# Optimization experiments

Measured on AMD Instinct MI355X. Metric: run time of the kernel, lower is better.

The kernel has to match this reference:

```python
import jax, jax.numpy as jnp
import numpy as np

LEVELS = ((64, 176), (32, 88), (16, 44), (8, 22))
S_TOTAL = sum(h * w for h, w in LEVELS)  # 14960
C = 128; HH = 8; HD = 16; R = 4; L = 4; P = 8
G = 32; PC_MIN = -4.0; PC_MAX = 4.0
NUM_CLASSES = 17; PROP = 3 + 3 + 4 + 1 + NUM_CLASSES  # 28


def _ln(x, g, b):
    m = x.mean(-1, keepdims=True)
    v = ((x - m) ** 2).mean(-1, keepdims=True)
    return (x - m) * jax.lax.rsqrt(v + 1e-5) * g + b


def setup_inputs() -> dict:
    key = jax.random.key(0)
    ks = jax.random.split(key, 20)
    B, N, CAM = 1, 1024, 6
    d = {}
    d['query'] = jax.random.normal(ks[0], (B, N, C), jnp.float32)
    d['gaussian_props'] = jax.random.normal(ks[1], (B, N, PROP), jnp.float32)
    d['ms_feats'] = jax.random.normal(ks[2], (B, CAM, S_TOTAL, C), jnp.float32)
    d['depth_maps'] = jax.random.uniform(ks[3], (B, CAM, 64, 176), jnp.float32, 0.5, 50.0)
    d['lidar2img'] = jax.random.normal(ks[4], (B, CAM, 4, 4), jnp.float32)
    d['img_h'] = 256
    d['img_w'] = 704
    w = lambda k, shp: jax.random.normal(k, shp, jnp.float32) * 0.02
    d['W_sc'] = w(ks[5], (3, 3, 3, C, C)); d['b_sc'] = jnp.zeros((C,), jnp.float32)
    d['sc_g'] = jnp.ones((C,), jnp.float32); d['sc_b'] = jnp.zeros((C,), jnp.float32)
    d['ref_off_w'] = w(ks[6], (C, R * 3)); d['ref_off_b'] = jnp.zeros((R * 3,), jnp.float32)
    d['off_w'] = w(ks[7], (C, HH * R * L * P * 2)); d['off_b'] = jnp.zeros((HH * R * L * P * 2,), jnp.float32)
    d['aw_w'] = w(ks[8], (C, HH * R * L * P)); d['aw_b'] = jnp.zeros((HH * R * L * P,), jnp.float32)
    d['val_w'] = w(ks[9], (C, C)); d['val_b'] = jnp.zeros((C,), jnp.float32)
    d['out_w'] = w(ks[10], (C, C)); d['out_b'] = jnp.zeros((C,), jnp.float32)
    d['an_g'] = jnp.ones((C,), jnp.float32); d['an_b'] = jnp.zeros((C,), jnp.float32)
    d['f1_w'] = w(ks[11], (C, 4 * C)); d['f1_b'] = jnp.zeros((4 * C,), jnp.float32)
    d['f2_w'] = w(ks[12], (4 * C, C)); d['f2_b'] = jnp.zeros((C,), jnp.float32)
    d['fn_g'] = jnp.ones((C,), jnp.float32); d['fn_b'] = jnp.zeros((C,), jnp.float32)
    d['p1_w'] = w(ks[13], (C, C)); d['p1_b'] = jnp.zeros((C,), jnp.float32)
    d['p2_w'] = w(ks[14], (C, PROP)); d['p2_b'] = jnp.zeros((PROP,), jnp.float32)
    return d


def _forward(query, gaussian_props, ms_feats, depth_maps, lidar2img,
             W_sc, b_sc, sc_g, sc_b, ref_off_w, ref_off_b, off_w, off_b,
             aw_w, aw_b, val_w, val_b, out_w, out_b, an_g, an_b,
             f1_w, f1_b, f2_w, f2_b, fn_g, fn_b, p1_w, p1_b, p2_w, p2_b,
             img_h, img_w):
    B, N, _ = query.shape
    CAM = ms_feats.shape[1]
    means = gaussian_props[..., :3]
    # ---- SparseConv3DBlock: scatter-mean voxelization, 3x3x3 conv, gather back ----
    vs = (PC_MAX - PC_MIN) / G
    vox = jnp.clip(jnp.floor((means - PC_MIN) / vs).astype(jnp.int32), 0, G - 1)
    flat = (vox[..., 0] * G + vox[..., 1]) * G + vox[..., 2]  # [B,N]
    bi = jnp.arange(B)[:, None]
    grid = jnp.zeros((B, G * G * G, C), query.dtype).at[bi, flat].add(query)
    cnt = jnp.zeros((B, G * G * G, 1), query.dtype).at[bi, flat].add(1.0)
    grid = (grid / jnp.maximum(cnt, 1.0)).reshape(B, G, G, G, C)
    grid = jax.lax.conv_general_dilated(grid, W_sc, (1, 1, 1), 'SAME',
                                        dimension_numbers=('NDHWC', 'DHWIO', 'NDHWC')) + b_sc
    grid = jax.nn.gelu(grid).reshape(B, G * G * G, C)
    query = _ln(query + grid[bi, flat], sc_g, sc_b)
    # ---- DeformableAttention3D ----
    fW = jnp.asarray(img_w, query.dtype); fH = jnp.asarray(img_h, query.dtype)
    ref3d = means[:, :, None, :] + (query @ ref_off_w + ref_off_b).reshape(B, N, R, 3)
    pts = jnp.concatenate([ref3d, jnp.ones_like(ref3d[..., :1])], -1)
    proj = jnp.einsum('bcij,bnrj->bcnri', lidar2img, pts)  # [B,CAM,N,R,4]
    z = proj[..., 2]; zc = jnp.maximum(z, 1e-5)
    u = proj[..., 0] / zc; v = proj[..., 1] / zc
    valid = (z > 1e-5) & (u >= 0) & (u < fW) & (v >= 0) & (v < fH)
    Hd, Wd = depth_maps.shape[2], depth_maps.shape[3]
    iu = jnp.clip((u / fW * Wd).astype(jnp.int32), 0, Wd - 1)
    iv = jnp.clip((v / fH * Hd).astype(jnp.int32), 0, Hd - 1)
    ds = jnp.take_along_axis(depth_maps.reshape(B, CAM, Hd * Wd),
                             (iv * Wd + iu).reshape(B, CAM, N * R), axis=2).reshape(B, CAM, N, R)
    wmask = jnp.exp(-jnp.abs(z - ds)) * valid.astype(query.dtype)  # [B,CAM,N,R]
    ref2 = jnp.stack([u / fW, v / fH], -1)  # [B,CAM,N,R,2]
    offs = (query @ off_w + off_b).reshape(B, N, HH, R, L, P, 2)
    attn = jax.nn.softmax((query @ aw_w + aw_b).reshape(B, N, HH, R * L * P), -1)
    attn = attn.reshape(B, N, HH, R, L, P)
    value = (ms_feats @ val_w + val_b).reshape(B, CAM, S_TOTAL, HH, HD)
    out = jnp.zeros((B, N, HH, HD), query.dtype)
    s0 = 0
    for l, (Hl, Wl) in enumerate(LEVELS):
        sz = Hl * Wl
        vl = value[:, :, s0:s0 + sz].transpose(0, 1, 3, 2, 4).reshape(B * CAM, HH, sz, HD)
        s0 += sz
        off_l = offs[:, :, :, :, l]  # [B,N,HH,R,P,2]
        loc = ref2[:, :, :, None, :, None, :] + off_l[:, None] / jnp.array([Wl, Hl], query.dtype)
        # loc: [B,CAM,N,HH,R,P,2] in normalized coords
        x = (loc[..., 0] * Wl - 0.5).transpose(0, 1, 3, 2, 4, 5).reshape(B * CAM, HH, N * R * P)
        y = (loc[..., 1] * Hl - 0.5).transpose(0, 1, 3, 2, 4, 5).reshape(B * CAM, HH, N * R * P)
        x0 = jnp.floor(x); y0 = jnp.floor(y); wx = x - x0; wy = y - y0
        x0i = jnp.clip(x0.astype(jnp.int32), 0, Wl - 1)
        x1i = jnp.clip(x0.astype(jnp.int32) + 1, 0, Wl - 1)
        y0i = jnp.clip(y0.astype(jnp.int32), 0, Hl - 1)
        y1i = jnp.clip(y0.astype(jnp.int32) + 1, 0, Hl - 1)
        g = lambda ix, iy: jnp.take_along_axis(vl, (iy * Wl + ix)[..., None], axis=2)
        samp = (((1 - wx) * (1 - wy))[..., None] * g(x0i, y0i)
                + (wx * (1 - wy))[..., None] * g(x1i, y0i)
                + ((1 - wx) * wy)[..., None] * g(x0i, y1i)
                + (wx * wy)[..., None] * g(x1i, y1i))  # [B*CAM,HH,N*R*P,HD]
        samp = samp.reshape(B, CAM, HH, N, R, P, HD)
        ws = attn[:, :, :, :, l, :][:, None].transpose(0, 1, 3, 2, 4, 5) * wmask[:, :, None, :, :, None]
        out = out + jnp.einsum('bchnrp,bchnrpd->bnhd', ws, samp)
    attn_out = out.reshape(B, N, C) @ out_w + out_b
    query = _ln(query + attn_out, an_g, an_b)
    query = _ln(query + (jax.nn.gelu(query @ f1_w + f1_b) @ f2_w + f2_b), fn_g, fn_b)
    props = gaussian_props + (jax.nn.gelu(query @ p1_w + p1_b) @ p2_w + p2_b)
    return query, props


def reference(query, gaussian_props, ms_feats, depth_maps, lidar2img,
              W_sc, b_sc, sc_g, sc_b, ref_off_w, ref_off_b, off_w, off_b,
              aw_w, aw_b, val_w, val_b, out_w, out_b, an_g, an_b,
              f1_w, f1_b, f2_w, f2_b, fn_g, fn_b, p1_w, p1_b, p2_w, p2_b,
              img_h, img_w):
    return _forward(query, gaussian_props, ms_feats, depth_maps, lidar2img,
                    W_sc, b_sc, sc_g, sc_b, ref_off_w, ref_off_b, off_w, off_b,
                    aw_w, aw_b, val_w, val_b, out_w, out_b, an_g, an_b,
                    f1_w, f1_b, f2_w, f2_b, fn_g, fn_b, p1_w, p1_b, p2_w, p2_b,
                    img_h, img_w)
```

## Files before the change

kernel.cpp:

```cpp
#include <hip/hip_runtime.h>
#include <hip/hip_bf16.h>
#include <math.h>

#define NQ    1024
#define CC    128
#define CAM   6
#define RR    4
#define LL    4
#define PP    8
#define HHD   8
#define HDD   16
#define GG    32
#define S_TOT 14960
#define PROPN 28
#define NTAP  27
#define MVAL  (CAM * S_TOT)
#define NVB   ((MVAL + 63) / 64)
#define NCVB  (8 * NTAP)

typedef __attribute__((ext_vector_type(8))) short bf16x8;
typedef __attribute__((ext_vector_type(4))) float f32x4;

__device__ __forceinline__ float gelu_tanh(float x) {
    return 0.5f * x * (1.0f + tanhf(0.7978845608028654f * (x + 0.044715f * x * x * x)));
}

__device__ __forceinline__ unsigned short f2bf(float f) {
    union { float f; unsigned int u; } x; x.f = f;
    unsigned int r = (x.u + 0x7FFFu + ((x.u >> 16) & 1u)) >> 16;
    return (unsigned short)r;
}

__device__ __forceinline__ float bf2f(short s) {
    union { unsigned int u; float f; } x;
    x.u = ((unsigned int)(unsigned short)s) << 16;
    return x.f;
}

__global__ void k_wt_scatter(const float* __restrict__ Wsc, unsigned short* __restrict__ WscT,
                             const float* __restrict__ valw, unsigned short* __restrict__ valwT,
                             const float* __restrict__ outw, unsigned short* __restrict__ outwT,
                             const float* __restrict__ p1w, unsigned short* __restrict__ p1wT,
                             const float* __restrict__ f1w, unsigned short* __restrict__ f1wT,
                             const float* __restrict__ f2w, unsigned short* __restrict__ f2wT,
                             const float* __restrict__ offw, unsigned short* __restrict__ offwT,
                             const float* __restrict__ aww, unsigned short* __restrict__ awwT,
                             const float* __restrict__ p2w, unsigned short* __restrict__ p2wT,
                             const float* __restrict__ p2b, float* __restrict__ p2bp,
                             const float* __restrict__ qin, const float* __restrict__ gp,
                             float* __restrict__ grid, float* __restrict__ cnt,
                             int* __restrict__ flatidx) {
    __shared__ float t[64][65];
    __shared__ int sflat[2];
    int z = blockIdx.z;
    int tid = threadIdx.x;

    if (z >= 63) {
        int half = tid >> 7, c = tid & 127;
        int n = ((z - 63) * 4 + (blockIdx.x * 2 + blockIdx.y)) * 2 + half;
        if (c == 0) {
            float mx = gp[n * PROPN + 0], my = gp[n * PROPN + 1], mz = gp[n * PROPN + 2];
            int vx = (int)floorf((mx + 4.0f) * 4.0f);
            int vy = (int)floorf((my + 4.0f) * 4.0f);
            int vz = (int)floorf((mz + 4.0f) * 4.0f);
            vx = min(max(vx, 0), GG - 1);
            vy = min(max(vy, 0), GG - 1);
            vz = min(max(vz, 0), GG - 1);
            int f = (vx * GG + vy) * GG + vz;
            sflat[half] = f;
            flatidx[n] = f;
            atomicAdd(&cnt[f], 1.0f);
        }
        __syncthreads();
        atomicAdd(&grid[(size_t)sflat[half] * CC + c], qin[(size_t)n * CC + c]);
        return;
    }

    int n0 = blockIdx.x * 64, k0 = blockIdx.y * 64;
    if (z == 62) {
#pragma unroll
        for (int it = 0; it < 16; ++it) {
            int idx = tid + it * 256;
            int r = idx >> 6, c = idx & 63;
            t[r][c] = (n0 + c < PROPN) ? p2w[(size_t)(k0 + r) * PROPN + n0 + c] : 0.f;
        }
        __syncthreads();
#pragma unroll
        for (int it = 0; it < 16; ++it) {
            int idx = tid + it * 256;
            int r = idx >> 6, c = idx & 63;
            p2wT[(size_t)(n0 + r) * 128 + k0 + c] = f2bf(t[c][r]);
        }
        if (blockIdx.x == 0 && blockIdx.y == 0 && tid < 128)
            p2bp[tid] = (tid < PROPN) ? p2b[tid] : 0.f;
        return;
    }
    const float* src; unsigned short* dst; int ss, ds;
    if (z < 27)       { src = Wsc + (size_t)z * 16384; dst = WscT + (size_t)z * 16384; ss = 128; ds = 128; }
    else if (z == 27) { src = valw; dst = valwT; ss = 128; ds = 128; }
    else if (z == 28) { src = outw; dst = outwT; ss = 128; ds = 128; }
    else if (z == 29) { src = p1w;  dst = p1wT;  ss = 128; ds = 128; }
    else if (z < 34)  { int q = z - 30; src = f1w + q * 128; dst = f1wT + (size_t)q * 16384; ss = 512;  ds = 128; }
    else if (z < 38)  { int q = z - 34; src = f2w + (size_t)q * 16384; dst = f2wT + q * 128; ss = 128;  ds = 512; }
    else if (z < 54)  { int q = z - 38; src = offw + q * 128; dst = offwT + (size_t)q * 16384; ss = 2048; ds = 128; }
    else              { int q = z - 54; src = aww + q * 128;  dst = awwT + (size_t)q * 16384; ss = 1024; ds = 128; }
#pragma unroll
    for (int it = 0; it < 16; ++it) {
        int idx = tid + it * 256;
        int r = idx >> 6, c = idx & 63;
        t[r][c] = src[(size_t)(k0 + r) * ss + n0 + c];
    }
    __syncthreads();
#pragma unroll
    for (int it = 0; it < 16; ++it) {
        int idx = tid + it * 256;
        int r = idx >> 6, c = idx & 63;
        dst[(size_t)(n0 + r) * ds + k0 + c] = f2bf(t[c][r]);
    }
}

union CVSm {
    struct { bf16x8 As[128 * 16]; bf16x8 Bs[128 * 16]; } c;
    struct { bf16x8 Bs[128 * 16]; unsigned short Os[64 * 128]; float sbias[128]; } v;
};
__global__ __launch_bounds__(256) void k_conv_val(
    const float* __restrict__ grid, const float* __restrict__ cnt,
    const int* __restrict__ flatidx, const unsigned short* __restrict__ WT,
    float* __restrict__ convacc27,
    const float* __restrict__ ms, const unsigned short* __restrict__ valwT,
    const float* __restrict__ valb, unsigned short* __restrict__ value)
{
    __shared__ CVSm sm;
    __shared__ int   nbase[128];
    __shared__ float nscale[128];
    int bx = blockIdx.x, tid = threadIdx.x;
    int lane = tid & 63, wv = tid >> 6;
    int r = lane & 15, q = lane >> 4;

    if (bx >= NCVB) {
        int vb = bx - NCVB;
        int m0 = vb * 64;
#pragma unroll
        for (int it = 0; it < 8; ++it) {
            int idx = tid + it * 256;
            int n = idx >> 4, c = idx & 15;
            sm.v.Bs[n * 16 + (c ^ (n & 15))] = *(const bf16x8*)(valwT + (size_t)n * 128 + c * 8);
        }
        if (tid < 128) sm.v.sbias[tid] = valb[tid];
        __syncthreads();

        int row = m0 + wv * 16 + r;
        int mg = min(row, MVAL - 1);
        const float* pA = ms + (size_t)mg * 128;

        f32x4 acc[8];
#pragma unroll
        for (int j = 0; j < 8; ++j)
#pragma unroll
            for (int e = 0; e < 4; ++e) acc[j][e] = 0.f;

#pragma unroll
        for (int ks = 0; ks < 4; ++ks) {
            const float* p = pA + ks * 32 + q * 8;
            float4 aa = *(const float4*)p;
            float4 bb = *(const float4*)(p + 4);
            bf16x8 af;
            af[0] = (short)f2bf(aa.x); af[1] = (short)f2bf(aa.y);
            af[2] = (short)f2bf(aa.z); af[3] = (short)f2bf(aa.w);
            af[4] = (short)f2bf(bb.x); af[5] = (short)f2bf(bb.y);
            af[6] = (short)f2bf(bb.z); af[7] = (short)f2bf(bb.w);
            bf16x8 bfr[8];
#pragma unroll
            for (int j = 0; j < 8; ++j)
                bfr[j] = sm.v.Bs[(j * 16 + r) * 16 + ((ks * 4 + q) ^ r)];
#pragma unroll
            for (int j = 0; j < 8; ++j)
                acc[j] = __builtin_amdgcn_mfma_f32_16x16x32_bf16(af, bfr[j], acc[j], 0, 0, 0);
        }

#pragma unroll
        for (int j = 0; j < 8; ++j)
#pragma unroll
            for (int e = 0; e < 4; ++e) {
                int rl = wv * 16 + q * 4 + e;
                sm.v.Os[rl * 128 + j * 16 + r] = f2bf(acc[j][e] + sm.v.sbias[j * 16 + r]);
            }
        __syncthreads();
#pragma unroll
        for (int it = 0; it < 2; ++it) {
            int idx = tid + it * 256;
            int rl = idx & 63, h = idx >> 6;
            int m = m0 + rl;
            if (m < MVAL) {
                int cam = m / S_TOT;
                int s = m - cam * S_TOT;
                int pos, HW, sb;
                if (s < 11264)      { pos = s;          HW = 11264; sb = 0; }
                else if (s < 14080) { pos = s - 11264;  HW = 2816;  sb = 11264; }
                else if (s < 14784) { pos = s - 14080;  HW = 704;   sb = 14080; }
                else                { pos = s - 14784;  HW = 176;   sb = 14784; }
                size_t dst = ((size_t)cam * S_TOT + sb) * CC
                           + (size_t)h * (HW * HDD) + (size_t)pos * HDD;
                *(bf16x8*)(value + dst)     = *(const bf16x8*)&sm.v.Os[rl * 128 + h * 16];
                *(bf16x8*)(value + dst + 8) = *(const bf16x8*)&sm.v.Os[rl * 128 + h * 16 + 8];
            }
        }
        return;
    }

    int tap = bx >> 3;
    int q0 = (bx & 7) * 128;
    int dz = tap / 9 - 1, dy = (tap / 3) % 3 - 1, dx = tap % 3 - 1;

    if (tid < 128) {
        int f = flatidx[q0 + tid];
        int nx = (f >> 10) + dz, ny = ((f >> 5) & 31) + dy, nz = (f & 31) + dx;
        bool ok = (nx >= 0 && nx < GG && ny >= 0 && ny < GG && nz >= 0 && nz < GG);
        int nf = ok ? (nx * GG + ny) * GG + nz : 0;
        nbase[tid] = nf;
        nscale[tid] = ok ? 1.0f / fmaxf(cnt[nf], 1.0f) : 0.f;
    }
    __syncthreads();
#pragma unroll
    for (int it = 0; it < 8; ++it) {
        int idx = tid + it * 256;
        int m = idx >> 4, c = idx & 15;
        const float* p = grid + (size_t)nbase[m] * CC + c * 8;
        float s = nscale[m];
        float4 a = *(const float4*)p;
        float4 b = *(const float4*)(p + 4);
        bf16x8 u;
        u[0] = (short)f2bf(a.x * s); u[1] = (short)f2bf(a.y * s);
        u[2] = (short)f2bf(a.z * s); u[3] = (short)f2bf(a.w * s);
        u[4] = (short)f2bf(b.x * s); u[5] = (short)f2bf(b.y * s);
        u[6] = (short)f2bf(b.z * s); u[7] = (short)f2bf(b.w * s);
        sm.c.As[m * 16 + (c ^ (m & 15))] = u;
    }
    const unsigned short* Wt = WT + (size_t)tap * CC * CC;
#pragma unroll
    for (int it = 0; it < 8; ++it) {
        int idx = tid + it * 256;
        int n = idx >> 4, c = idx & 15;
        bf16x8 w = *(const bf16x8*)(Wt + (size_t)n * CC + c * 8);
        sm.c.Bs[n * 16 + (c ^ (n & 15))] = w;
    }
    __syncthreads();

    int wr = (wv >> 1) * 64, wc = (wv & 1) * 64;
    f32x4 acc[4][4];
#pragma unroll
    for (int i = 0; i < 4; ++i)
#pragma unroll
        for (int j = 0; j < 4; ++j)
#pragma unroll
            for (int e = 0; e < 4; ++e) acc[i][j][e] = 0.f;
#pragma unroll
    for (int ks = 0; ks < 4; ++ks) {
        bf16x8 bfr[4];
#pragma unroll
        for (int j = 0; j < 4; ++j)
            bfr[j] = sm.c.Bs[(wc + j * 16 + r) * 16 + ((ks * 4 + q) ^ r)];
#pragma unroll
        for (int i = 0; i < 4; ++i) {
            bf16x8 af = sm.c.As[(wr + i * 16 + r) * 16 + ((ks * 4 + q) ^ r)];
#pragma unroll
            for (int j = 0; j < 4; ++j)
                acc[i][j] = __builtin_amdgcn_mfma_f32_16x16x32_bf16(af, bfr[j], acc[i][j], 0, 0, 0);
        }
    }
    float* dst = convacc27 + (size_t)tap * NQ * CC;
#pragma unroll
    for (int i = 0; i < 4; ++i)
#pragma unroll
        for (int e = 0; e < 4; ++e) {
            int m = q0 + wr + i * 16 + q * 4 + e;
#pragma unroll
            for (int j = 0; j < 4; ++j) {
                int col = wc + j * 16 + r;
                dst[(size_t)m * CC + col] = acc[i][j][e];
            }
        }
}

__global__ void k_ln_conv_proj(const float* __restrict__ a, const float* __restrict__ convacc27,
                               const float* __restrict__ bconv,
                               const float* __restrict__ g, const float* __restrict__ be,
                               float* __restrict__ out, unsigned short* __restrict__ outbf,
                               const float* __restrict__ refw, const float* __restrict__ refb,
                               const float* __restrict__ gp, const float* __restrict__ l2i,
                               const float* __restrict__ depth,
                               const int* __restrict__ ih, const int* __restrict__ iw,
                               float* __restrict__ wm, float* __restrict__ r2u,
                               float* __restrict__ r2v) {
    int n = blockIdx.x, c = threadIdx.x;
    float apart = 0.f;
#pragma unroll
    for (int t = 0; t < NTAP; ++t) apart += convacc27[((size_t)t * NQ + n) * CC + c];
    float x = a[n * CC + c] + gelu_tanh(apart + bconv[c]);
    __shared__ float w4[4];
    __shared__ float qrow[CC];
    __shared__ float ro[12];
    float s = x;
#pragma unroll
    for (int d = 1; d < 64; d <<= 1) s += __shfl_xor(s, d);
    if ((c & 63) == 0) w4[c >> 6] = s;
    __syncthreads();
    float m = (w4[0] + w4[1]) * (1.0f / CC);
    float dd = x - m;
    float v = dd * dd;
#pragma unroll
    for (int d = 1; d < 64; d <<= 1) v += __shfl_xor(v, d);
    if ((c & 63) == 0) w4[2 + (c >> 6)] = v;
    __syncthreads();
    float var = (w4[2] + w4[3]) * (1.0f / CC);
    float qv = dd * rsqrtf(var + 1e-5f) * g[c] + be[c];
    out[n * CC + c] = qv;
    outbf[n * CC + c] = f2bf(qv);
    qrow[c] = qv;
    __syncthreads();
    if (c < 12) {
        float sacc = refb[c];
#pragma unroll 4
        for (int k = 0; k < 128; ++k) sacc += qrow[k] * refw[k * 12 + c];
        ro[c] = sacc;
    }
    __syncthreads();
    if (c < 24) {
        int cam = c >> 2, r = c & 3;
        float fH = (float)(*ih), fW = (float)(*iw);
        const float* M = l2i + cam * 16;
        float px = gp[n * PROPN + 0] + ro[r * 3 + 0];
        float py = gp[n * PROPN + 1] + ro[r * 3 + 1];
        float pz = gp[n * PROPN + 2] + ro[r * 3 + 2];
        float p0 = M[0] * px + M[1] * py + M[2]  * pz + M[3];
        float p1 = M[4] * px + M[5] * py + M[6]  * pz + M[7];
        float p2 = M[8] * px + M[9] * py + M[10] * pz + M[11];
        float zc = fmaxf(p2, 1e-5f);
        float u = p0 / zc, vv = p1 / zc;
        bool valid = (p2 > 1e-5f) && (u >= 0.f) && (u < fW) && (vv >= 0.f) && (vv < fH);
        int iu = min(max((int)(u / fW * 176.f), 0), 175);
        int iv = min(max((int)(vv / fH * 64.f), 0), 63);
        float ds = depth[cam * 64 * 176 + iv * 176 + iu];
        int o = cam * (NQ * RR) + n * RR + r;
        wm[o]  = valid ? expf(-fabsf(p2 - ds)) : 0.f;
        r2u[o] = u / fW;
        r2v[o] = vv / fH;
    }
}

__global__ __launch_bounds__(256) void k_qhead(
    const unsigned short* __restrict__ Abf,
    const unsigned short* __restrict__ offwT, const float* __restrict__ offb,
    unsigned short* __restrict__ offsb,
    const unsigned short* __restrict__ awwT, const float* __restrict__ awb,
    unsigned short* __restrict__ attn)
{
    __shared__ bf16x8 Bs[128 * 16];
    int bx = blockIdx.x, tid = threadIdx.x;
    int lane = tid & 63, wv = tid >> 6;
    int r = lane & 15, q = lane >> 4;
    bool isoff = bx < 16;
    int n0 = (isoff ? bx : (bx - 16)) * 128;
    const unsigned short* WT = isoff ? offwT : awwT;
    int m0 = blockIdx.y * 128;
    int mw = m0 + wv * 32;

#pragma unroll
    for (int it = 0; it < 8; ++it) {
        int idx = tid + it * 256;
        int n = idx >> 4, c = idx & 15;
        Bs[n * 16 + (c ^ (n & 15))] = *(const bf16x8*)(WT + (size_t)(n0 + n) * 128 + c * 8);
    }
    __syncthreads();

    f32x4 acc[2][8];
#pragma unroll
    for (int i = 0; i < 2; ++i)
#pragma unroll
        for (int j = 0; j < 8; ++j)
#pragma unroll
            for (int e = 0; e < 4; ++e) acc[i][j][e] = 0.f;

#pragma unroll
    for (int ks = 0; ks < 4; ++ks) {
        bf16x8 af[2];
#pragma unroll
        for (int i = 0; i < 2; ++i)
            af[i] = *(const bf16x8*)(Abf + (size_t)(mw + i * 16 + r) * 128 + (ks * 4 + q) * 8);
#pragma unroll
        for (int j = 0; j < 8; ++j) {
            bf16x8 b = Bs[(j * 16 + r) * 16 + ((ks * 4 + q) ^ r)];
#pragma unroll
            for (int i = 0; i < 2; ++i)
                acc[i][j] = __builtin_amdgcn_mfma_f32_16x16x32_bf16(af[i], b, acc[i][j], 0, 0, 0);
        }
    }

    float bia[8];
    const float* bsrc = isoff ? offb : awb;
#pragma unroll
    for (int j = 0; j < 8; ++j) bia[j] = bsrc[n0 + j * 16 + r];

    if (isoff) {
#pragma unroll
        for (int i = 0; i < 2; ++i)
#pragma unroll
            for (int e = 0; e < 4; ++e) {
                int m = mw + i * 16 + q * 4 + e;
                unsigned short* orow = offsb + (size_t)m * 2048 + n0;
#pragma unroll
                for (int j = 0; j < 8; ++j)
                    orow[j * 16 + r] = f2bf(acc[i][j][e] + bia[j]);
            }
    } else {
#pragma unroll
        for (int i = 0; i < 2; ++i)
#pragma unroll
            for (int e = 0; e < 4; ++e) {
                float mx = -1e30f;
#pragma unroll
                for (int j = 0; j < 8; ++j) mx = fmaxf(mx, acc[i][j][e] + bia[j]);
#pragma unroll
                for (int d = 1; d < 16; d <<= 1) mx = fmaxf(mx, __shfl_xor(mx, d));
                float ex[8];
                float sum = 0.f;
#pragma unroll
                for (int j = 0; j < 8; ++j) { ex[j] = expf(acc[i][j][e] + bia[j] - mx); sum += ex[j]; }
#pragma unroll
                for (int d = 1; d < 16; d <<= 1) sum += __shfl_xor(sum, d);
                float inv = 1.0f / sum;
                int m = mw + i * 16 + q * 4 + e;
                unsigned short* orow = attn + (size_t)m * 1024 + n0;
#pragma unroll
                for (int j = 0; j < 8; ++j)
                    orow[j * 16 + r] = f2bf(ex[j] * inv);
            }
    }
}

__global__ __launch_bounds__(512) void k_sample(
                         const unsigned short* __restrict__ value,
                         const unsigned short* __restrict__ offsb,
                         const unsigned short* __restrict__ attn,
                         const float* __restrict__ wm,
                         const float* __restrict__ r2u, const float* __restrict__ r2v,
                         float* __restrict__ sampout) {
    const int Wl_[4] = {176, 88, 44, 22};
    const int Hl_[4] = {64, 32, 16, 8};
    const int s0_[4] = {0, 11264, 14080, 14784};
    int n = blockIdx.x, tid = threadIdx.x;
    __shared__ float s_attn[1024];
    __shared__ float s_offs[2048];
    __shared__ float s_wm[24], s_ru[24], s_rv[24];
    __shared__ float part[HHD][HDD];

    if (tid < 128) {
        bf16x8 v = *(const bf16x8*)(attn + (size_t)n * 1024 + tid * 8);
#pragma unroll
        for (int d = 0; d < 8; ++d) s_attn[tid * 8 + d] = bf2f(v[d]);
    }
    if (tid < 256) {
        bf16x8 v = *(const bf16x8*)(offsb + (size_t)n * 2048 + tid * 8);
#pragma unroll
        for (int d = 0; d < 8; ++d) s_offs[tid * 8 + d] = bf2f(v[d]);
    }
    if (tid < 24) {
        int cam = tid >> 2, r = tid & 3;
        int o = cam * (NQ * RR) + n * RR + r;
        s_wm[tid] = wm[o]; s_ru[tid] = r2u[o]; s_rv[tid] = r2v[o];
    }
    __syncthreads();

    int half = tid >> 8;
    int t8 = tid & 255;
    int h = t8 >> 5, slot = t8 & 31;
    int l = slot >> 3, p = slot & 7;
    int Wl = Wl_[l], Hl = Hl_[l];
    float fWl = (float)Wl, fHl = (float)Hl;
    size_t planeC = (size_t)s0_[l] * CC + (size_t)h * (Hl * Wl * HDD);
    float acc[16];
#pragma unroll
    for (int d = 0; d < 16; ++d) acc[d] = 0.f;

    for (int cr = half * 12; cr < half * 12 + 12; ++cr) {
        int cam = cr >> 2, r = cr & 3;
        float ws = s_attn[h * 128 + r * 32 + l * 8 + p] * s_wm[cr];
        if (ws == 0.f) continue;
        float ox = s_offs[h * 256 + r * 64 + l * 16 + p * 2 + 0];
        float oy = s_offs[h * 256 + r * 64 + l * 16 + p * 2 + 1];
        float x = s_ru[cr] * fWl + ox - 0.5f;
        float y = s_rv[cr] * fHl + oy - 0.5f;
        float xf = floorf(x), yf = floorf(y);
        float wx = x - xf, wy = y - yf;
        int x0 = min(max((int)xf, 0), Wl - 1);
        int x1 = min(max((int)xf + 1, 0), Wl - 1);
        int y0 = min(max((int)yf, 0), Hl - 1);
        int y1 = min(max((int)yf + 1, 0), Hl - 1);
        const unsigned short* base = value + (size_t)cam * S_TOT * CC + planeC;
        const unsigned short* p00 = base + (size_t)(y0 * Wl + x0) * HDD;
        const unsigned short* p01 = base + (size_t)(y0 * Wl + x1) * HDD;
        const unsigned short* p10 = base + (size_t)(y1 * Wl + x0) * HDD;
        const unsigned short* p11 = base + (size_t)(y1 * Wl + x1) * HDD;
        float w00 = ws * (1.f - wx) * (1.f - wy);
        float w01 = ws * wx * (1.f - wy);
        float w10 = ws * (1.f - wx) * wy;
        float w11 = ws * wx * wy;
        bf16x8 va0 = *(const bf16x8*)p00, va1 = *(const bf16x8*)(p00 + 8);
        bf16x8 vb0 = *(const bf16x8*)p01, vb1 = *(const bf16x8*)(p01 + 8);
        bf16x8 vc0 = *(const bf16x8*)p10, vc1 = *(const bf16x8*)(p10 + 8);
        bf16x8 vd0 = *(const bf16x8*)p11, vd1 = *(const bf16x8*)(p11 + 8);
#pragma unroll
        for (int d = 0; d < 8; ++d)
            acc[d] += w00 * bf2f(va0[d]) + w01 * bf2f(vb0[d]) + w10 * bf2f(vc0[d]) + w11 * bf2f(vd0[d]);
#pragma unroll
        for (int d = 0; d < 8; ++d)
            acc[8 + d] += w00 * bf2f(va1[d]) + w01 * bf2f(vb1[d]) + w10 * bf2f(vc1[d]) + w11 * bf2f(vd1[d]);
    }

#pragma unroll
    for (int d = 0; d < 16; ++d) {
        float a = acc[d];
#pragma unroll
        for (int s = 16; s >= 1; s >>= 1) a += __shfl_xor(a, s, 32);
        acc[d] = a;
    }
    if (half == 1 && slot == 0) {
#pragma unroll
        for (int d = 0; d < 16; ++d) part[h][d] = acc[d];
    }
    __syncthreads();
    if (half == 0 && slot == 0) {
#pragma unroll
        for (int d = 0; d < 16; ++d)
            sampout[(size_t)n * CC + h * HDD + d] = acc[d] + part[h][d];
    }
}

__global__ __launch_bounds__(512) void k_tail(
    const float* __restrict__ sampout,
    const unsigned short* __restrict__ outwT, const float* __restrict__ outb,
    const float* __restrict__ q1, const float* __restrict__ ang, const float* __restrict__ anb,
    const unsigned short* __restrict__ f1wT, const float* __restrict__ f1b,
    const unsigned short* __restrict__ f2wT, const float* __restrict__ f2b,
    const float* __restrict__ fng, const float* __restrict__ fnb,
    const unsigned short* __restrict__ p1wT, const float* __restrict__ p1b,
    const unsigned short* __restrict__ p2wT, const float* __restrict__ p2bp,
    const float* __restrict__ gp, float* __restrict__ outq, float* __restrict__ outp)
{
    __shared__ bf16x8 As[16 * 16];
    __shared__ bf16x8 Aff[16 * 64];
    __shared__ float xrow[16 * 128];
    __shared__ float q2s[16 * 128];
    unsigned short* Affu = (unsigned short*)Aff;
    unsigned short* As2u = (unsigned short*)Aff;
    int tid = threadIdx.x, m0 = blockIdx.x * 16;
    int lane = tid & 63, wv = tid >> 6;
    int wc = wv * 16;
    int r = lane & 15, q = lane >> 4;
    int lrow = tid >> 5, ls = tid & 31;

    bf16x8 b1[4];
#pragma unroll
    for (int ks = 0; ks < 4; ++ks)
        b1[ks] = *(const bf16x8*)(outwT + (size_t)(wc + r) * 128 + (ks * 4 + q) * 8);

    if (tid < 256) {
        int m = tid >> 4, c = tid & 15;
        const float* p = sampout + (size_t)(m0 + m) * 128 + c * 8;
        float4 a = *(const float4*)p;
        float4 b = *(const float4*)(p + 4);
        bf16x8 u;
        u[0] = (short)f2bf(a.x); u[1] = (short)f2bf(a.y);
        u[2] = (short)f2bf(a.z); u[3] = (short)f2bf(a.w);
        u[4] = (short)f2bf(b.x); u[5] = (short)f2bf(b.y);
        u[6] = (short)f2bf(b.z); u[7] = (short)f2bf(b.w);
        As[m * 16 + (c ^ m)] = u;
    }
    __syncthreads();

    f32x4 acc;
    bf16x8 a4[4];
#pragma unroll
    for (int ks = 0; ks < 4; ++ks) a4[ks] = As[r * 16 + ((ks * 4 + q) ^ r)];
#pragma unroll
    for (int e = 0; e < 4; ++e) acc[e] = 0.f;
#pragma unroll
    for (int ks = 0; ks < 4; ++ks)
        acc = __builtin_amdgcn_mfma_f32_16x16x32_bf16(a4[ks], b1[ks], acc, 0, 0, 0);
#pragma unroll
    for (int e = 0; e < 4; ++e) {
        int ml = q * 4 + e;
        int cl = wc + r;
        xrow[ml * 128 + cl] = acc[e] + outb[cl] + q1[(size_t)(m0 + ml) * 128 + cl];
    }
    __syncthreads();

    {
        float* xr = xrow + lrow * 128;
        float sum = 0.f;
#pragma unroll
        for (int e = ls; e < 128; e += 32) sum += xr[e];
#pragma unroll
        for (int d = 16; d; d >>= 1) sum += __shfl_xor(sum, d, 32);
        float mean = sum * (1.0f / 128.0f);
        float var = 0.f;
#pragma unroll
        for (int e = ls; e < 128; e += 32) { float dd = xr[e] - mean; var += dd * dd; }
#pragma unroll
        for (int d = 16; d; d >>= 1) var += __shfl_xor(var, d, 32);
        float rstd = rsqrtf(var * (1.0f / 128.0f) + 1e-5f);
#pragma unroll
        for (int e = ls; e < 128; e += 32)
            q2s[lrow * 128 + e] = (xr[e] - mean) * rstd * ang[e] + anb[e];
    }
    __syncthreads();
    if (tid < 256) {
        int m = tid >> 4, c = tid & 15;
        const float* p = q2s + m * 128 + c * 8;
        bf16x8 u;
#pragma unroll
        for (int d = 0; d < 8; ++d) u[d] = (short)f2bf(p[d]);
        As[m * 16 + (c ^ m)] = u;
    }
    __syncthreads();

#pragma unroll
    for (int ks = 0; ks < 4; ++ks) a4[ks] = As[r * 16 + ((ks * 4 + q) ^ r)];
    bf16x8 bcur[4];
#pragma unroll
    for (int ks = 0; ks < 4; ++ks)
        bcur[ks] = *(const bf16x8*)(f1wT + (size_t)(wc + r) * 128 + (ks * 4 + q) * 8);
#pragma unroll
    for (int nt = 0; nt < 4; ++nt) {
        bf16x8 bnx[4];
        if (nt < 3) {
#pragma unroll
            for (int ks = 0; ks < 4; ++ks)
                bnx[ks] = *(const bf16x8*)(f1wT + (size_t)(nt + 1) * 16384
                                            + (size_t)(wc + r) * 128 + (ks * 4 + q) * 8);
        }
#pragma unroll
        for (int e = 0; e < 4; ++e) acc[e] = 0.f;
#pragma unroll
        for (int ks = 0; ks < 4; ++ks)
            acc = __builtin_amdgcn_mfma_f32_16x16x32_bf16(a4[ks], bcur[ks], acc, 0, 0, 0);
#pragma unroll
        for (int e = 0; e < 4; ++e) {
            int ml = q * 4 + e;
            int col = nt * 128 + wc + r;
            float v = gelu_tanh(acc[e] + f1b[col]);
            Affu[(ml * 64 + ((col >> 3) ^ ml)) * 8 + (col & 7)] = f2bf(v);
        }
        if (nt < 3) {
#pragma unroll
            for (int ks = 0; ks < 4; ++ks) bcur[ks] = bnx[ks];
        }
    }
    __syncthreads();

#pragma unroll
    for (int e = 0; e < 4; ++e) acc[e] = 0.f;
#pragma unroll
    for (int ks = 0; ks < 4; ++ks)
        bcur[ks] = *(const bf16x8*)(f2wT + (size_t)(wc + r) * 512 + (ks * 4 + q) * 8);
#pragma unroll
    for (int kc = 0; kc < 4; ++kc) {
        bf16x8 bnx[4];
        if (kc < 3) {
#pragma unroll
            for (int ks = 0; ks < 4; ++ks)
                bnx[ks] = *(const bf16x8*)(f2wT + (size_t)(wc + r) * 512
                                            + ((kc + 1) * 16 + ks * 4 + q) * 8);
        }
#pragma unroll
        for (int ks = 0; ks < 4; ++ks) {
            bf16x8 af = Aff[r * 64 + ((kc * 16 + ks * 4 + q) ^ r)];
            acc = __builtin_amdgcn_mfma_f32_16x16x32_bf16(af, bcur[ks], acc, 0, 0, 0);
        }
        if (kc < 3) {
#pragma unroll
            for (int ks = 0; ks < 4; ++ks) bcur[ks] = bnx[ks];
        }
    }
#pragma unroll
    for (int e = 0; e < 4; ++e) {
        int ml = q * 4 + e;
        int cl = wc + r;
        xrow[ml * 128 + cl] = acc[e] + f2b[cl] + q2s[ml * 128 + cl];
    }
    __syncthreads();

    {
        float* xr = xrow + lrow * 128;
        float sum = 0.f;
#pragma unroll
        for (int e = ls; e < 128; e += 32) sum += xr[e];
#pragma unroll
        for (int d = 16; d; d >>= 1) sum += __shfl_xor(sum, d, 32);
        float mean = sum * (1.0f / 128.0f);
        float var = 0.f;
#pragma unroll
        for (int e = ls; e < 128; e += 32) { float dd = xr[e] - mean; var += dd * dd; }
#pragma unroll
        for (int d = 16; d; d >>= 1) var += __shfl_xor(var, d, 32);
        float rstd = rsqrtf(var * (1.0f / 128.0f) + 1e-5f);
        float* oq = outq + (size_t)(m0 + lrow) * 128;
#pragma unroll
        for (int e = ls; e < 128; e += 32) {
            float v = (xr[e] - mean) * rstd * fng[e] + fnb[e];
            oq[e] = v;
            q2s[lrow * 128 + e] = v;
        }
    }
    __syncthreads();
    if (tid < 256) {
        int m = tid >> 4, c = tid & 15;
        const float* p = q2s + m * 128 + c * 8;
        bf16x8 u;
#pragma unroll
        for (int d = 0; d < 8; ++d) u[d] = (short)f2bf(p[d]);
        As[m * 16 + (c ^ m)] = u;
    }
    __syncthreads();

#pragma unroll
    for (int ks = 0; ks < 4; ++ks) a4[ks] = As[r * 16 + ((ks * 4 + q) ^ r)];
#pragma unroll
    for (int ks = 0; ks < 4; ++ks)
        bcur[ks] = *(const bf16x8*)(p1wT + (size_t)(wc + r) * 128 + (ks * 4 + q) * 8);
#pragma unroll
    for (int ks = 0; ks < 4; ++ks)
        b1[ks] = *(const bf16x8*)(p2wT + (size_t)(wc + r) * 128 + (ks * 4 + q) * 8);
#pragma unroll
    for (int e = 0; e < 4; ++e) acc[e] = 0.f;
#pragma unroll
    for (int ks = 0; ks < 4; ++ks)
        acc = __builtin_amdgcn_mfma_f32_16x16x32_bf16(a4[ks], bcur[ks], acc, 0, 0, 0);
#pragma unroll
    for (int e = 0; e < 4; ++e) {
        int ml = q * 4 + e;
        int cl = wc + r;
        float v = gelu_tanh(acc[e] + p1b[cl]);
        As2u[(ml * 16 + ((cl >> 3) ^ ml)) * 8 + (cl & 7)] = f2bf(v);
    }
    __syncthreads();

#pragma unroll
    for (int e = 0; e < 4; ++e) acc[e] = 0.f;
#pragma unroll
    for (int ks = 0; ks < 4; ++ks) {
        bf16x8 af = Aff[r * 16 + ((ks * 4 + q) ^ r)];
        acc = __builtin_amdgcn_mfma_f32_16x16x32_bf16(af, b1[ks], acc, 0, 0, 0);
    }
#pragma unroll
    for (int e = 0; e < 4; ++e) {
        int m = m0 + q * 4 + e;
        int cl = wc + r;
        if (cl < PROPN)
            outp[(size_t)m * PROPN + cl] = acc[e] + p2bp[cl] + gp[(size_t)m * PROPN + cl];
    }
}

extern "C" void kernel_launch(void* const* d_in, const int* in_sizes, int n_in,
                              void* d_out, int out_size, void* d_ws, size_t ws_size,
                              hipStream_t stream) {
    const float* query = (const float*)d_in[0];
    const float* gp    = (const float*)d_in[1];
    const float* ms    = (const float*)d_in[2];
    const float* depth = (const float*)d_in[3];
    const float* l2i   = (const float*)d_in[4];
    const int*   ih    = (const int*)d_in[5];
    const int*   iw    = (const int*)d_in[6];
    const float* Wsc   = (const float*)d_in[7];
    const float* bsc   = (const float*)d_in[8];
    const float* scg   = (const float*)d_in[9];
    const float* scb   = (const float*)d_in[10];
    const float* refw  = (const float*)d_in[11];
    const float* refb  = (const float*)d_in[12];
    const float* offw  = (const float*)d_in[13];
    const float* offbi = (const float*)d_in[14];
    const float* aww   = (const float*)d_in[15];
    const float* awb   = (const float*)d_in[16];
    const float* valw  = (const float*)d_in[17];
    const float* valb  = (const float*)d_in[18];
    const float* outw  = (const float*)d_in[19];
    const float* outb  = (const float*)d_in[20];
    const float* ang   = (const float*)d_in[21];
    const float* anb   = (const float*)d_in[22];
    const float* f1w   = (const float*)d_in[23];
    const float* f1b   = (const float*)d_in[24];
    const float* f2w   = (const float*)d_in[25];
    const float* f2b   = (const float*)d_in[26];
    const float* fng   = (const float*)d_in[27];
    const float* fnb   = (const float*)d_in[28];
    const float* p1w   = (const float*)d_in[29];
    const float* p1b   = (const float*)d_in[30];
    const float* p2w   = (const float*)d_in[31];
    const float* p2b   = (const float*)d_in[32];

    float* outq = (float*)d_out;
    float* outp = outq + NQ * CC;

    float* ws = (float*)d_ws;
    size_t o = 0;
    float* grid    = ws + o; o += (size_t)GG * GG * GG * CC;
    float* cnt     = ws + o; o += GG * GG * GG;
    size_t zero_floats = o;
    int*   flatidx = (int*)(ws + o); o += NQ;
    float* convacc27 = ws + o; o += (size_t)NTAP * NQ * CC;
    float* q1      = ws + o; o += NQ * CC;
    float* wm      = ws + o; o += CAM * NQ * RR;
    float* r2u     = ws + o; o += CAM * NQ * RR;
    float* r2v     = ws + o; o += CAM * NQ * RR;
    float* sampout = ws + o; o += NQ * CC;
    float* p2bp    = ws + o; o += 128;
    unsigned short* u16base = (unsigned short*)(ws + o);
    size_t uo = 0;
    unsigned short* value = u16base + uo; uo += (size_t)CAM * S_TOT * CC;
    unsigned short* offsb = u16base + uo; uo += (size_t)NQ * 2048;
    unsigned short* attn  = u16base + uo; uo += (size_t)NQ * 1024;
    unsigned short* q1bf  = u16base + uo; uo += (size_t)NQ * CC;
    unsigned short* offwT = u16base + uo; uo += (size_t)2048 * 128;
    unsigned short* awwT  = u16base + uo; uo += (size_t)1024 * 128;
    unsigned short* valwT = u16base + uo; uo += 128 * 128;
    unsigned short* outwT = u16base + uo; uo += 128 * 128;
    unsigned short* f1wT  = u16base + uo; uo += 512 * 128;
    unsigned short* f2wT  = u16base + uo; uo += 128 * 512;
    unsigned short* p1wT  = u16base + uo; uo += 128 * 128;
    unsigned short* p2wT  = u16base + uo; uo += 128 * 128;
    unsigned short* WscT  = u16base + uo; uo += (size_t)27 * 128 * 128;
    (void)ws_size; (void)in_sizes; (void)n_in; (void)out_size;

    hipMemsetAsync(ws, 0, zero_floats * sizeof(float), stream);

    k_wt_scatter<<<dim3(2, 2, 63 + 128), 256, 0, stream>>>(
        Wsc, WscT, valw, valwT, outw, outwT, p1w, p1wT, f1w, f1wT, f2w, f2wT,
        offw, offwT, aww, awwT, p2w, p2wT, p2b, p2bp,
        query, gp, grid, cnt, flatidx);

    k_conv_val<<<dim3(NCVB + NVB), 256, 0, stream>>>(
        grid, cnt, flatidx, WscT, convacc27,
        ms, valwT, valb, value);

    k_ln_conv_proj<<<NQ, CC, 0, stream>>>(query, convacc27, bsc, scg, scb, q1, q1bf,
                                          refw, refb, gp, l2i, depth, ih, iw, wm, r2u, r2v);

    k_qhead<<<dim3(24, 8), 256, 0, stream>>>(q1bf, offwT, offbi, offsb, awwT, awb, attn);

    k_sample<<<NQ, 512, 0, stream>>>(value, offsb, attn, wm, r2u, r2v, sampout);

    k_tail<<<64, 512, 0, stream>>>(sampout, outwT, outb, q1, ang, anb,
                                   f1wT, f1b, f2wT, f2b, fng, fnb,
                                   p1wT, p1b, p2wT, p2bp, gp, outq, outp);
}
```

Before: 221.4 us.

## Redistribute weight transposes into downstream kernels and retile qhead and ref projection

The first kernel now transposes only the conv weights. The value-projection weights are converted to bf16 inline inside the value blocks, and the offset/attention and tail weight transposes run as extra blocks in the conv/value and LN kernels. This shortens the critical first kernel and hides the transposes behind other work. The qhead GEMM tile drops from 128 to 64 rows to double its block count, and the 12-output reference projection is spread over 96 threads with shuffle reductions. The cost is a heavier prologue in every value block, since each one re-reads and converts the fp32 value weights.

Measured after the change: 230.2 us. 4.0% more time.

```diff
diff --git a/kernel.cpp b/kernel.cpp
--- a/kernel.cpp
+++ b/kernel.cpp
@@ -38,15 +38,6 @@
 }
 
 __global__ void k_wt_scatter(const float* __restrict__ Wsc, unsigned short* __restrict__ WscT,
-                             const float* __restrict__ valw, unsigned short* __restrict__ valwT,
-                             const float* __restrict__ outw, unsigned short* __restrict__ outwT,
-                             const float* __restrict__ p1w, unsigned short* __restrict__ p1wT,
-                             const float* __restrict__ f1w, unsigned short* __restrict__ f1wT,
-                             const float* __restrict__ f2w, unsigned short* __restrict__ f2wT,
-                             const float* __restrict__ offw, unsigned short* __restrict__ offwT,
-                             const float* __restrict__ aww, unsigned short* __restrict__ awwT,
-                             const float* __restrict__ p2w, unsigned short* __restrict__ p2wT,
-                             const float* __restrict__ p2b, float* __restrict__ p2bp,
                              const float* __restrict__ qin, const float* __restrict__ gp,
                              float* __restrict__ grid, float* __restrict__ cnt,
                              int* __restrict__ flatidx) {
@@ -55,9 +46,9 @@
     int z = blockIdx.z;
     int tid = threadIdx.x;
 
-    if (z >= 63) {
+    if (z >= 27) {
         int half = tid >> 7, c = tid & 127;
-        int n = ((z - 63) * 4 + (blockIdx.x * 2 + blockIdx.y)) * 2 + half;
+        int n = ((z - 27) * 4 + (blockIdx.x * 2 + blockIdx.y)) * 2 + half;
         if (c == 0) {
             float mx = gp[n * PROPN + 0], my = gp[n * PROPN + 1], mz = gp[n * PROPN + 2];
             int vx = (int)floorf((mx + 4.0f) * 4.0f);
@@ -77,58 +68,36 @@
     }
 
     int n0 = blockIdx.x * 64, k0 = blockIdx.y * 64;
-    if (z == 62) {
-#pragma unroll
-        for (int it = 0; it < 16; ++it) {
-            int idx = tid + it * 256;
-            int r = idx >> 6, c = idx & 63;
-            t[r][c] = (n0 + c < PROPN) ? p2w[(size_t)(k0 + r) * PROPN + n0 + c] : 0.f;
-        }
-        __syncthreads();
-#pragma unroll
-        for (int it = 0; it < 16; ++it) {
-            int idx = tid + it * 256;
-            int r = idx >> 6, c = idx & 63;
-            p2wT[(size_t)(n0 + r) * 128 + k0 + c] = f2bf(t[c][r]);
-        }
-        if (blockIdx.x == 0 && blockIdx.y == 0 && tid < 128)
-            p2bp[tid] = (tid < PROPN) ? p2b[tid] : 0.f;
-        return;
-    }
-    const float* src; unsigned short* dst; int ss, ds;
-    if (z < 27)       { src = Wsc + (size_t)z * 16384; dst = WscT + (size_t)z * 16384; ss = 128; ds = 128; }
-    else if (z == 27) { src = valw; dst = valwT; ss = 128; ds = 128; }
-    else if (z == 28) { src = outw; dst = outwT; ss = 128; ds = 128; }
-    else if (z == 29) { src = p1w;  dst = p1wT;  ss = 128; ds = 128; }
-    else if (z < 34)  { int q = z - 30; src = f1w + q * 128; dst = f1wT + (size_t)q * 16384; ss = 512;  ds = 128; }
-    else if (z < 38)  { int q = z - 34; src = f2w + (size_t)q * 16384; dst = f2wT + q * 128; ss = 128;  ds = 512; }
-    else if (z < 54)  { int q = z - 38; src = offw + q * 128; dst = offwT + (size_t)q * 16384; ss = 2048; ds = 128; }
-    else              { int q = z - 54; src = aww + q * 128;  dst = awwT + (size_t)q * 16384; ss = 1024; ds = 128; }
+    const float* src = Wsc + (size_t)z * 16384;
+    unsigned short* dst = WscT + (size_t)z * 16384;
 #pragma unroll
     for (int it = 0; it < 16; ++it) {
         int idx = tid + it * 256;
         int r = idx >> 6, c = idx & 63;
-        t[r][c] = src[(size_t)(k0 + r) * ss + n0 + c];
+        t[r][c] = src[(size_t)(k0 + r) * 128 + n0 + c];
     }
     __syncthreads();
 #pragma unroll
     for (int it = 0; it < 16; ++it) {
         int idx = tid + it * 256;
         int r = idx >> 6, c = idx & 63;
-        dst[(size_t)(n0 + r) * ds + k0 + c] = f2bf(t[c][r]);
+        dst[(size_t)(n0 + r) * 128 + k0 + c] = f2bf(t[c][r]);
     }
 }
 
 union CVSm {
     struct { bf16x8 As[128 * 16]; bf16x8 Bs[128 * 16]; } c;
     struct { bf16x8 Bs[128 * 16]; unsigned short Os[64 * 128]; float sbias[128]; } v;
+    float t[64][65];
 };
 __global__ __launch_bounds__(256) void k_conv_val(
     const float* __restrict__ grid, const float* __restrict__ cnt,
     const int* __restrict__ flatidx, const unsigned short* __restrict__ WT,
     float* __restrict__ convacc27,
-    const float* __restrict__ ms, const unsigned short* __restrict__ valwT,
-    const float* __restrict__ valb, unsigned short* __restrict__ value)
+    const float* __restrict__ ms, const float* __restrict__ valw,
+    const float* __restrict__ valb, unsigned short* __restrict__ value,
+    const float* __restrict__ offw, unsigned short* __restrict__ offwT,
+    const float* __restrict__ aww, unsigned short* __restrict__ awwT)
 {
     __shared__ CVSm sm;
     __shared__ int   nbase[128];
@@ -137,14 +106,40 @@
     int lane = tid & 63, wv = tid >> 6;
     int r = lane & 15, q = lane >> 4;
 
+    if (bx >= NCVB + NVB) {
+        int tb = bx - (NCVB + NVB);
+        int plane = tb >> 2, tile = tb & 3;
+        int n0 = (tile >> 1) * 64, k0 = (tile & 1) * 64;
+        const float* src; unsigned short* dst; int ss;
+        if (plane < 16) { src = offw + plane * 128;       dst = offwT + (size_t)plane * 16384;       ss = 2048; }
+        else            { src = aww + (plane - 16) * 128; dst = awwT + (size_t)(plane - 16) * 16384; ss = 1024; }
+#pragma unroll
+        for (int it = 0; it < 16; ++it) {
+            int idx = tid + it * 256;
+            int rr = idx >> 6, c = idx & 63;
+            sm.t[rr][c] = src[(size_t)(k0 + rr) * ss + n0 + c];
+        }
+        __syncthreads();
+#pragma unroll
+        for (int it = 0; it < 16; ++it) {
+            int idx = tid + it * 256;
+            int rr = idx >> 6, c = idx & 63;
+            dst[(size_t)(n0 + rr) * 128 + k0 + c] = f2bf(sm.t[c][rr]);
+        }
+        return;
+    }
+
     if (bx >= NCVB) {
         int vb = bx - NCVB;
         int m0 = vb * 64;
-#pragma unroll
-        for (int it = 0; it < 8; ++it) {
+        unsigned int* Bsw = (unsigned int*)sm.v.Bs;
+#pragma unroll
+        for (int it = 0; it < 32; ++it) {
             int idx = tid + it * 256;
-            int n = idx >> 4, c = idx & 15;
-            sm.v.Bs[n * 16 + (c ^ (n & 15))] = *(const bf16x8*)(valwT + (size_t)n * 128 + c * 8);
+            int k = (idx >> 7) * 2, nn = idx & 127;
+            unsigned int lo = f2bf(valw[k * 128 + nn]);
+            unsigned int hi = f2bf(valw[(k + 1) * 128 + nn]);
+            Bsw[(nn * 16 + ((k >> 3) ^ (nn & 15))) * 4 + ((k >> 1) & 3)] = lo | (hi << 16);
         }
         if (tid < 128) sm.v.sbias[tid] = valb[tid];
         __syncthreads();
@@ -291,15 +286,66 @@
                                const float* __restrict__ depth,
                                const int* __restrict__ ih, const int* __restrict__ iw,
                                float* __restrict__ wm, float* __restrict__ r2u,
-                               float* __restrict__ r2v) {
-    int n = blockIdx.x, c = threadIdx.x;
-    float apart = 0.f;
-#pragma unroll
-    for (int t = 0; t < NTAP; ++t) apart += convacc27[((size_t)t * NQ + n) * CC + c];
-    float x = a[n * CC + c] + gelu_tanh(apart + bconv[c]);
+                               float* __restrict__ r2v,
+                               const float* __restrict__ outw, unsigned short* __restrict__ outwT,
+                               const float* __restrict__ p1w, unsigned short* __restrict__ p1wT,
+                               const float* __restrict__ f1w, unsigned short* __restrict__ f1wT,
+                               const float* __restrict__ f2w, unsigned short* __restrict__ f2wT,
+                               const float* __restrict__ p2w, unsigned short* __restrict__ p2wT,
+                               const float* __restrict__ p2b, float* __restrict__ p2bp) {
+    __shared__ float t[64][65];
     __shared__ float w4[4];
     __shared__ float qrow[CC];
     __shared__ float ro[12];
+    int bx = blockIdx.x, c = threadIdx.x;
+
+    if (bx >= NQ) {
+        int tb = bx - NQ;
+        int plane = tb >> 2, tile = tb & 3;
+        int n0 = (tile >> 1) * 64, k0 = (tile & 1) * 64;
+        if (plane == 10) {
+#pragma unroll
+            for (int it = 0; it < 32; ++it) {
+                int idx = c + it * 128;
+                int r = idx >> 6, cc = idx & 63;
+                t[r][cc] = (n0 + cc < PROPN) ? p2w[(size_t)(k0 + r) * PROPN + n0 + cc] : 0.f;
+            }
+            __syncthreads();
+#pragma unroll
+            for (int it = 0; it < 32; ++it) {
+                int idx = c + it * 128;
+                int r = idx >> 6, cc = idx & 63;
+                p2wT[(size_t)(n0 + r) * 128 + k0 + cc] = f2bf(t[cc][r]);
+            }
+            if (tile == 0) p2bp[c] = (c < PROPN) ? p2b[c] : 0.f;
+            return;
+        }
+        const float* src; unsigned short* dst; int ss, ds;
+        if (plane == 0)      { src = outw; dst = outwT; ss = 128; ds = 128; }
+        else if (plane == 1) { src = p1w;  dst = p1wT;  ss = 128; ds = 128; }
+        else if (plane < 6)  { int qq = plane - 2; src = f1w + qq * 128; dst = f1wT + (size_t)qq * 16384; ss = 512; ds = 128; }
+        else                 { int qq = plane - 6; src = f2w + (size_t)qq * 16384; dst = f2wT + qq * 128; ss = 128; ds = 512; }
+#pragma unroll
+        for (int it = 0; it < 32; ++it) {
+            int idx = c + it * 128;
+            int r = idx >> 6, cc = idx & 63;
+            t[r][cc] = src[(size_t)(k0 + r) * ss + n0 + cc];
+        }
+        __syncthreads();
+#pragma unroll
+        for (int it = 0; it < 32; ++it) {
+            int idx = c + it * 128;
+            int r = idx >> 6, cc = idx & 63;
+            dst[(size_t)(n0 + r) * ds + k0 + cc] = f2bf(t[cc][r]);
+        }
+        return;
+    }
+
+    int n = bx;
+    float apart = 0.f;
+#pragma unroll
+    for (int tt = 0; tt < NTAP; ++tt) apart += convacc27[((size_t)tt * NQ + n) * CC + c];
+    float x = a[n * CC + c] + gelu_tanh(apart + bconv[c]);
     float s = x;
 #pragma unroll
     for (int d = 1; d < 64; d <<= 1) s += __shfl_xor(s, d);
@@ -318,11 +364,17 @@
     outbf[n * CC + c] = f2bf(qv);
     qrow[c] = qv;
     __syncthreads();
-    if (c < 12) {
-        float sacc = refb[c];
-#pragma unroll 4
-        for (int k = 0; k < 128; ++k) sacc += qrow[k] * refw[k * 12 + c];
-        ro[c] = sacc;
+    if (c < 96) {
+        int dg = c >> 3, ll = c & 7;
+        float sacc = 0.f;
+#pragma unroll
+        for (int k = 0; k < 16; ++k) {
+            int kk = ll * 16 + k;
+            sacc += qrow[kk] * refw[kk * 12 + dg];
+        }
+#pragma unroll
+        for (int d = 4; d; d >>= 1) sacc += __shfl_xor(sacc, d, 8);
+        if (ll == 0) ro[dg] = sacc + refb[dg];
     }
     __syncthreads();
     if (c < 24) {
@@ -362,8 +414,8 @@
     bool isoff = bx < 16;
     int n0 = (isoff ? bx : (bx - 16)) * 128;
     const unsigned short* WT = isoff ? offwT : awwT;
-    int m0 = blockIdx.y * 128;
-    int mw = m0 + wv * 32;
+    int m0 = blockIdx.y * 64;
+    int mw = m0 + wv * 16;
 
 #pragma unroll
     for (int it = 0; it < 8; ++it) {
@@ -373,26 +425,19 @@
     }
     __syncthreads();
 
-    f32x4 acc[2][8];
-#pragma unroll
-    for (int i = 0; i < 2; ++i)
-#pragma unroll
-        for (int j = 0; j < 8; ++j)
-#pragma unroll
-            for (int e = 0; e < 4; ++e) acc[i][j][e] = 0.f;
+    f32x4 acc[8];
+#pragma unroll
+    for (int j = 0; j < 8; ++j)
+#pragma unroll
+        for (int e = 0; e < 4; ++e) acc[j][e] = 0.f;
 
 #pragma unroll
     for (int ks = 0; ks < 4; ++ks) {
-        bf16x8 af[2];
-#pragma unroll
-        for (int i = 0; i < 2; ++i)
-            af[i] = *(const bf16x8*)(Abf + (size_t)(mw + i * 16 + r) * 128 + (ks * 4 + q) * 8);
+        bf16x8 af = *(const bf16x8*)(Abf + (size_t)(mw + r) * 128 + (ks * 4 + q) * 8);
 #pragma unroll
         for (int j = 0; j < 8; ++j) {
             bf16x8 b = Bs[(j * 16 + r) * 16 + ((ks * 4 + q) ^ r)];
-#pragma unroll
-            for (int i = 0; i < 2; ++i)
-                acc[i][j] = __builtin_amdgcn_mfma_f32_16x16x32_bf16(af[i], b, acc[i][j], 0, 0, 0);
+            acc[j] = __builtin_amdgcn_mfma_f32_16x16x32_bf16(af, b, acc[j], 0, 0, 0);
         }
     }
 
@@ -403,38 +448,34 @@
 
     if (isoff) {
 #pragma unroll
-        for (int i = 0; i < 2; ++i)
-#pragma unroll
-            for (int e = 0; e < 4; ++e) {
-                int m = mw + i * 16 + q * 4 + e;
-                unsigned short* orow = offsb + (size_t)m * 2048 + n0;
-#pragma unroll
-                for (int j = 0; j < 8; ++j)
-                    orow[j * 16 + r] = f2bf(acc[i][j][e] + bia[j]);
-            }
+        for (int e = 0; e < 4; ++e) {
+            int m = mw + q * 4 + e;
+            unsigned short* orow = offsb + (size_t)m * 2048 + n0;
+#pragma unroll
+            for (int j = 0; j < 8; ++j)
+                orow[j * 16 + r] = f2bf(acc[j][e] + bia[j]);
+        }
     } else {
 #pragma unroll
-        for (int i = 0; i < 2; ++i)
-#pragma unroll
-            for (int e = 0; e < 4; ++e) {
-                float mx = -1e30f;
-#pragma unroll
-                for (int j = 0; j < 8; ++j) mx = fmaxf(mx, acc[i][j][e] + bia[j]);
-#pragma unroll
-                for (int d = 1; d < 16; d <<= 1) mx = fmaxf(mx, __shfl_xor(mx, d));
-                float ex[8];
-                float sum = 0.f;
-#pragma unroll
-                for (int j = 0; j < 8; ++j) { ex[j] = expf(acc[i][j][e] + bia[j] - mx); sum += ex[j]; }
-#pragma unroll
-                for (int d = 1; d < 16; d <<= 1) sum += __shfl_xor(sum, d);
-                float inv = 1.0f / sum;
-                int m = mw + i * 16 + q * 4 + e;
-                unsigned short* orow = attn + (size_t)m * 1024 + n0;
-#pragma unroll
-                for (int j = 0; j < 8; ++j)
-                    orow[j * 16 + r] = f2bf(ex[j] * inv);
-            }
+        for (int e = 0; e < 4; ++e) {
+            float mx = -1e30f;
+#pragma unroll
+            for (int j = 0; j < 8; ++j) mx = fmaxf(mx, acc[j][e] + bia[j]);
+#pragma unroll
+            for (int d = 1; d < 16; d <<= 1) mx = fmaxf(mx, __shfl_xor(mx, d));
+            float ex[8];
+            float sum = 0.f;
+#pragma unroll
+            for (int j = 0; j < 8; ++j) { ex[j] = expf(acc[j][e] + bia[j] - mx); sum += ex[j]; }
+#pragma unroll
+            for (int d = 1; d < 16; d <<= 1) sum += __shfl_xor(sum, d);
+            float inv = 1.0f / sum;
+            int m = mw + q * 4 + e;
+            unsigned short* orow = attn + (size_t)m * 1024 + n0;
+#pragma unroll
+            for (int j = 0; j < 8; ++j)
+                orow[j * 16 + r] = f2bf(ex[j] * inv);
+        }
     }
 }
 
@@ -725,9 +766,10 @@
 
 #pragma unroll
     for (int ks = 0; ks < 4; ++ks) a4[ks] = As[r * 16 + ((ks * 4 + q) ^ r)];
+    bf16x8 bcur2[4];
 #pragma unroll
     for (int ks = 0; ks < 4; ++ks)
-        bcur[ks] = *(const bf16x8*)(p1wT + (size_t)(wc + r) * 128 + (ks * 4 + q) * 8);
+        bcur2[ks] = *(const bf16x8*)(p1wT + (size_t)(wc + r) * 128 + (ks * 4 + q) * 8);
 #pragma unroll
     for (int ks = 0; ks < 4; ++ks)
         b1[ks] = *(const bf16x8*)(p2wT + (size_t)(wc + r) * 128 + (ks * 4 + q) * 8);
@@ -735,7 +777,7 @@
     for (int e = 0; e < 4; ++e) acc[e] = 0.f;
 #pragma unroll
     for (int ks = 0; ks < 4; ++ks)
-        acc = __builtin_amdgcn_mfma_f32_16x16x32_bf16(a4[ks], bcur[ks], acc, 0, 0, 0);
+        acc = __builtin_amdgcn_mfma_f32_16x16x32_bf16(a4[ks], bcur2[ks], acc, 0, 0, 0);
 #pragma unroll
     for (int e = 0; e < 4; ++e) {
         int ml = q * 4 + e;
@@ -822,7 +864,6 @@
     unsigned short* q1bf  = u16base + uo; uo += (size_t)NQ * CC;
     unsigned short* offwT = u16base + uo; uo += (size_t)2048 * 128;
     unsigned short* awwT  = u16base + uo; uo += (size_t)1024 * 128;
-    unsigned short* valwT = u16base + uo; uo += 128 * 128;
     unsigned short* outwT = u16base + uo; uo += 128 * 128;
     unsigned short* f1wT  = u16base + uo; uo += 512 * 128;
     unsigned short* f2wT  = u16base + uo; uo += 128 * 512;
@@ -833,19 +874,20 @@
 
     hipMemsetAsync(ws, 0, zero_floats * sizeof(float), stream);
 
-    k_wt_scatter<<<dim3(2, 2, 63 + 128), 256, 0, stream>>>(
-        Wsc, WscT, valw, valwT, outw, outwT, p1w, p1wT, f1w, f1wT, f2w, f2wT,
-        offw, offwT, aww, awwT, p2w, p2wT, p2b, p2bp,
-        query, gp, grid, cnt, flatidx);
-
-    k_conv_val<<<dim3(NCVB + NVB), 256, 0, stream>>>(
+    k_wt_scatter<<<dim3(2, 2, 27 + 128), 256, 0, stream>>>(
+        Wsc, WscT, query, gp, grid, cnt, flatidx);
+
+    k_conv_val<<<dim3(NCVB + NVB + 96), 256, 0, stream>>>(
         grid, cnt, flatidx, WscT, convacc27,
-        ms, valwT, valb, value);
-
-    k_ln_conv_proj<<<NQ, CC, 0, stream>>>(query, convacc27, bsc, scg, scb, q1, q1bf,
-                                          refw, refb, gp, l2i, depth, ih, iw, wm, r2u, r2v);
-
-    k_qhead<<<dim3(24, 8), 256, 0, stream>>>(q1bf, offwT, offbi, offsb, awwT, awb, attn);
+        ms, valw, valb, value,
+        offw, offwT, aww, awwT);
+
+    k_ln_conv_proj<<<NQ + 44, CC, 0, stream>>>(
+        query, convacc27, bsc, scg, scb, q1, q1bf,
+        refw, refb, gp, l2i, depth, ih, iw, wm, r2u, r2v,
+        outw, outwT, p1w, p1wT, f1w, f1wT, f2w, f2wT, p2w, p2wT, p2b, p2bp);
+
+    k_qhead<<<dim3(24, 16), 256, 0, stream>>>(q1bf, offwT, offbi, offsb, awwT, awb, attn);
 
     k_sample<<<NQ, 512, 0, stream>>>(value, offsb, attn, wm, r2u, r2v, sampout);
 
```
